# Kernel tuning notes

Measured on AMD Instinct MI355X. Metric: run time of the kernel, lower is better.

The kernel has to match this reference:

```python
import jax, jax.numpy as jnp
import numpy as np

N = 50000; IN_DIM = 128; HID = 128; T = 4; R = 3; E = 500000

def setup_inputs() -> dict:
    key = jax.random.key(0)
    ks = jax.random.split(key, 20)
    def nrm(k, shape, s):
        return jax.random.normal(k, shape, jnp.float32) * s
    s_in = 1.0 / float(np.sqrt(IN_DIM)); s_h = 1.0 / float(np.sqrt(HID))
    return {
        'feat_seq': nrm(ks[0], (T, N, IN_DIM), 1.0),
        'src': jax.random.randint(ks[1], (T, R, E), 0, N, jnp.int32),
        'dst': jax.random.randint(ks[2], (T, R, E), 0, N, jnp.int32),
        'ew': jax.random.uniform(ks[3], (T, R, E), jnp.float32),
        'W_in': nrm(ks[4], (IN_DIM, HID), s_in), 'b_in': jnp.zeros((HID,), jnp.float32),
        'W1': nrm(ks[5], (R, HID, HID), s_h), 'b1': jnp.zeros((R, HID), jnp.float32),
        'W2': nrm(ks[6], (R, HID, HID), s_h), 'b2': jnp.zeros((R, HID), jnp.float32),
        'q1': nrm(ks[7], (HID,), 1.0), 'q2': nrm(ks[8], (HID,), 1.0),
        'ln1_g': jnp.ones((HID,), jnp.float32), 'ln1_b': jnp.zeros((HID,), jnp.float32),
        'ln2_g': jnp.ones((HID,), jnp.float32), 'ln2_b': jnp.zeros((HID,), jnp.float32),
        'gWih': nrm(ks[9], (HID, 3 * HID), s_h), 'gbih': jnp.zeros((3 * HID,), jnp.float32),
        'gWhh': nrm(ks[10], (HID, 3 * HID), s_h), 'gbhh': jnp.zeros((3 * HID,), jnp.float32),
        'temp_q': nrm(ks[11], (HID,), 1.0),
        'tW1': nrm(ks[12], (IN_DIM, HID), s_in), 'tb1': jnp.zeros((HID,), jnp.float32),
        'tW2': nrm(ks[13], (HID, HID), s_h), 'tb2': jnp.zeros((HID,), jnp.float32),
        'cW1': nrm(ks[14], (3 * HID, HID), 1.0 / float(np.sqrt(3 * HID))), 'cb1': jnp.zeros((HID,), jnp.float32),
        'cW2': nrm(ks[15], (HID, 1), s_h), 'cb2': jnp.zeros((1,), jnp.float32),
    }

def _ln(x, g, b):
    m = x.mean(-1, keepdims=True)
    v = ((x - m) ** 2).mean(-1, keepdims=True)
    return (x - m) * jax.lax.rsqrt(v + 1e-5) * g + b

def _rel_attn(stack, q):
    # stack: [R,N,H]; tanh-softmax attention over relations
    score = jnp.einsum('rnh,h->rn', jnp.tanh(stack), q)
    alpha = jax.nn.softmax(score, axis=0)
    return jnp.einsum('rn,rnh->nh', alpha, stack)

def _conv(x, s, d, w, Wr, br):
    # DGL GraphConv norm='right' with edge_weight: mean-by-in-degree weighted SpMM
    msg = w[:, None] * x[s]                                   # [E,H]
    agg = jax.ops.segment_sum(msg, d, num_segments=N)
    deg = jax.ops.segment_sum(jnp.ones_like(w), d, num_segments=N)
    return (agg / jnp.maximum(deg, 1.0)[:, None]) @ Wr + br

def reference(feat_seq, src, dst, ew, W_in, b_in, W1, b1, W2, b2, q1, q2, ln1_g, ln1_b, ln2_g, ln2_b, gWih, gbih, gWhh, gbhh, temp_q, tW1, tb1, tW2, tb2, cW1, cb1, cW2, cb2):
    conv_all = jax.vmap(_conv, in_axes=(None, 0, 0, 0, 0, 0))
    def spatial(x, s, d, w):
        h0 = jax.nn.relu(x @ W_in + b_in)
        h1 = _ln(h0 + jax.nn.relu(_rel_attn(conv_all(h0, s, d, w, W1, b1), q1)), ln1_g, ln1_b)
        h2 = _ln(h1 + jax.nn.relu(_rel_attn(conv_all(h1, s, d, w, W2, b2), q2)), ln2_g, ln2_b)
        return h2
    hs = jnp.stack([spatial(feat_seq[t], src[t], dst[t], ew[t]) for t in range(T)], axis=0)  # [T,N,H]
    def gru_step(h, x):
        gi = x @ gWih + gbih
        gh = h @ gWhh + gbhh
        ir, iz, inn = jnp.split(gi, 3, axis=-1)
        hr, hz, hn = jnp.split(gh, 3, axis=-1)
        r = jax.nn.sigmoid(ir + hr)
        zg = jax.nn.sigmoid(iz + hz)
        n = jnp.tanh(inn + r * hn)
        hnew = (1.0 - zg) * n + zg * h
        return hnew, hnew
    _, outs = jax.lax.scan(gru_step, jnp.zeros((N, HID), feat_seq.dtype), hs)  # [T,N,H]
    out = jnp.transpose(outs, (1, 0, 2))                       # [N,T,H]
    last = out[:, -1, :]
    t_score = jnp.einsum('nth,h->nt', jnp.tanh(out), temp_q)
    t_alpha = jax.nn.softmax(t_score, axis=1)
    attn = jnp.einsum('nt,nth->nh', t_alpha, out)
    tab = jax.nn.relu(jax.nn.relu(feat_seq[-1] @ tW1 + tb1) @ tW2 + tb2)
    z = jnp.concatenate([last, attn, tab], axis=-1)
    return (jax.nn.relu(z @ cW1 + cb1) @ cW2 + cb2)[:, 0]       # [N]
```

## Files before the change

kernel.cpp:

```cpp
#include <hip/hip_runtime.h>
#include <hip/hip_bf16.h>
#include <math.h>

#define NN 50000
#define TT 4
#define RR 3
#define EE 500000

typedef __attribute__((ext_vector_type(8))) short bf16x8;
typedef __attribute__((ext_vector_type(4))) float f32x4;

__device__ inline unsigned short f2b(float f)
{
    union { __hip_bfloat16 h; unsigned short u; } cv;
    cv.h = __float2bfloat16(f);
    return cv.u;
}
__device__ inline float b2f(unsigned short u)
{
    union { unsigned int u; float f; } cv;
    cv.u = ((unsigned int)u) << 16;
    return cv.f;
}
__device__ inline bf16x8 pack8(float4 a, float4 b)
{
    bf16x8 r;
    r[0] = (short)f2b(a.x); r[1] = (short)f2b(a.y); r[2] = (short)f2b(a.z); r[3] = (short)f2b(a.w);
    r[4] = (short)f2b(b.x); r[5] = (short)f2b(b.y); r[6] = (short)f2b(b.z); r[7] = (short)f2b(b.w);
    return r;
}


__global__ __launch_bounds__(256)
void diag_kernel(float* __restrict__ out, float v)
{
    int i = blockIdx.x * 256 + threadIdx.x;
    if (i < NN) out[i] = v;
}


__global__ __launch_bounds__(256)
void wswz_kernel(const float* __restrict__ W, unsigned short* __restrict__ dst, int C, int S)
{
    int idx = blockIdx.x * 256 + threadIdx.x;
    int per = 128 * C;
    if (idx >= S * per) return;
    int s = idx / per, rem = idx - s * per;
    int j = rem & 7;
    int lane = (rem >> 3) & 63;
    int blk = rem >> 9;
    int ncg = C >> 4;
    int kc = blk / ncg, cg = blk - kc * ncg;
    int k = kc * 32 + (lane >> 4) * 8 + j;
    int c = cg * 16 + (lane & 15);
    dst[idx] = f2b(W[(size_t)s * 128 * C + (size_t)k * C + c]);
}


__global__ __launch_bounds__(256)
void count_kernel(const int* __restrict__ dst, int* __restrict__ cnt)
{
    int g = blockIdx.y;
    int e = blockIdx.x * 256 + threadIdx.x;
    if (e >= EE) return;
    int d = dst[(size_t)g * EE + e];
    atomicAdd(&cnt[(size_t)g * NN + d], 1);
}

__global__ __launch_bounds__(1024)
void scan_kernel(int* __restrict__ cnt, int* __restrict__ rows)
{
    int g = blockIdx.x;
    int tid = threadIdx.x;
    const int CH = (NN + 1023) / 1024;
    int s0 = tid * CH;
    int s1 = s0 + CH; if (s1 > NN) s1 = NN;
    int* c = cnt + (size_t)g * NN;
    int* ro = rows + (size_t)g * (NN + 1);
    int sum = 0;
    for (int i = s0; i < s1; ++i) sum += c[i];
    __shared__ int sd[1024];
    sd[tid] = sum;
    __syncthreads();
    for (int off = 1; off < 1024; off <<= 1) {
        int v = 0;
        if (tid >= off) v = sd[tid - off];
        __syncthreads();
        sd[tid] += v;
        __syncthreads();
    }
    int total = sd[1023];
    int prefix = (tid == 0) ? 0 : sd[tid - 1];
    for (int i = s0; i < s1; ++i) {
        int cv = c[i];
        ro[i] = prefix;
        c[i] = prefix;
        prefix += cv;
    }
    if (tid == 0) ro[NN] = total;
}

__global__ __launch_bounds__(256)
void fill_kernel(const int* __restrict__ src, const int* __restrict__ dst,
                 const float* __restrict__ ew, int* __restrict__ cur,
                 int2* __restrict__ srcw)
{
    int g = blockIdx.y;
    int e = blockIdx.x * 256 + threadIdx.x;
    if (e >= EE) return;
    size_t idx = (size_t)g * EE + e;
    int d = dst[idx];
    int pos = atomicAdd(&cur[(size_t)g * NN + d], 1);
    int2 p;
    p.x = src[idx];
    p.y = __float_as_int(ew[idx]);
    srcw[(size_t)g * EE + pos] = p;
}


__global__ __launch_bounds__(256)
void agg16_kernel(const unsigned short* __restrict__ x16,
                  const int2* __restrict__ srcw,
                  const int* __restrict__ rows,
                  unsigned short* __restrict__ agg16)
{
    int wid = (blockIdx.x * 256 + threadIdx.x) >> 6;
    int lane = threadIdx.x & 63;
    if (wid >= RR * NN) return;
    int r = wid / NN;
    int n = wid - r * NN;
    const int* rs = rows + (size_t)r * (NN + 1);
    int e0 = rs[n], e1 = rs[n + 1];
    const int2* sw = srcw + (size_t)r * EE;
    const int co = lane * 2;
    float ax = 0.f, ay = 0.f;
    for (int e = e0; e < e1; e += 16) {
        int2 p[16];
        unsigned int v[16];
#pragma unroll
        for (int i = 0; i < 16; ++i) {
            int idx = (e + i < e1) ? e + i : e1 - 1;
            p[i] = sw[idx];
        }
#pragma unroll
        for (int i = 0; i < 16; ++i)
            v[i] = *(const unsigned int*)(x16 + (size_t)p[i].x * 128 + co);
#pragma unroll
        for (int i = 0; i < 16; ++i) {
            float w = (e + i < e1) ? __int_as_float(p[i].y) : 0.f;
            ax += w * b2f((unsigned short)(v[i] & 0xffffu));
            ay += w * b2f((unsigned short)(v[i] >> 16));
        }
    }
    float inv = 1.0f / fmaxf((float)(e1 - e0), 1.0f);
    unsigned int o = (unsigned int)f2b(ax * inv) | ((unsigned int)f2b(ay * inv) << 16);
    *(unsigned int*)(agg16 + ((size_t)r * NN + n) * 128 + co) = o;
}


__global__ __launch_bounds__(256)
void mmb(const void* in, int in_bf16, long in_zs, int ldin,
         const unsigned short* __restrict__ Ws, long w_zs,
         const float* __restrict__ bias, long b_zs,
         float* out, long out_zs, int ldout,
         unsigned short* out16, long out16_zs,
         int rows, int act)
{
    const int tid = threadIdx.x;
    const int wv = tid >> 6, l = tid & 63;
    const int z = blockIdx.z;
    const int r0 = blockIdx.x * 64 + wv * 16;
    const int lk = (l >> 4) * 8;
    int rowA = r0 + (l & 15);
    int rowc = rowA < rows ? rowA : rows - 1;

    bf16x8 a[4];
    if (in_bf16) {
        const unsigned short* inb = (const unsigned short*)in + (size_t)z * in_zs
                                    + (size_t)rowc * ldin + lk;
#pragma unroll
        for (int kc = 0; kc < 4; ++kc) {
            uint4 u = *(const uint4*)(inb + kc * 32);
            a[kc] = *(bf16x8*)&u;
        }
    } else {
        const float* inf = (const float*)in + (size_t)z * in_zs
                           + (size_t)rowc * ldin + lk;
#pragma unroll
        for (int kc = 0; kc < 4; ++kc) {
            float4 u0 = *(const float4*)(inf + kc * 32);
            float4 u1 = *(const float4*)(inf + kc * 32 + 4);
            a[kc] = pack8(u0, u1);
        }
    }

    const unsigned short* Wz = Ws + (size_t)z * w_zs;
    const float* bz = bias + (size_t)z * b_zs;
    float* oz = out ? out + (size_t)z * out_zs : (float*)0;
    unsigned short* o16z = out16 ? out16 + (size_t)z * out16_zs : (unsigned short*)0;
    const int colbase = l & 15;
    const int rbase = r0 + (l >> 4) * 4;

#pragma unroll
    for (int cg = 0; cg < 8; ++cg) {
        f32x4 acc = {0.f, 0.f, 0.f, 0.f};
#pragma unroll
        for (int kc = 0; kc < 4; ++kc) {
            uint4 bu = *(const uint4*)(Wz + ((size_t)(kc * 8 + cg) * 64 + l) * 8);
            acc = __builtin_amdgcn_mfma_f32_16x16x32_bf16(a[kc], *(bf16x8*)&bu, acc, 0, 0, 0);
        }
        int col = cg * 16 + colbase;
        float bvv = bz[col];
#pragma unroll
        for (int j = 0; j < 4; ++j) {
            int gr = rbase + j;
            if (gr >= rows) continue;
            float v = acc[j] + bvv;
            if (act) v = fmaxf(v, 0.f);
            if (oz) oz[(size_t)gr * ldout + col] = v;
            if (o16z) o16z[(size_t)gr * 128 + col] = f2b(v);
        }
    }
}


__global__ __launch_bounds__(256)
void grub_all(const float* x, float* h,
              const unsigned short* __restrict__ Wis, const float* __restrict__ bi,
              const unsigned short* __restrict__ Whs, const float* __restrict__ bh,
              float* outs)
{
    const int tid = threadIdx.x;
    const int wv = tid >> 6, l = tid & 63;
    const int r0 = blockIdx.x * 64 + wv * 16;
    const int lk = (l >> 4) * 8;
    int rowA = r0 + (l & 15);
    int rowc = rowA < NN ? rowA : NN - 1;

    bf16x8 ax[4], hx[4];
    {
        const float* bx = x + (size_t)rowc * 128 + lk;
        const float* bhp = h + (size_t)rowc * 128 + lk;
#pragma unroll
        for (int kc = 0; kc < 4; ++kc) {
            ax[kc] = pack8(*(const float4*)(bx + kc * 32), *(const float4*)(bx + kc * 32 + 4));
            hx[kc] = pack8(*(const float4*)(bhp + kc * 32), *(const float4*)(bhp + kc * 32 + 4));
        }
    }
    const int colbase = l & 15;
    const int rbase = r0 + (l >> 4) * 4;

#pragma unroll
    for (int cg = 0; cg < 8; ++cg) {
        f32x4 air = {0.f,0.f,0.f,0.f}, ahr = {0.f,0.f,0.f,0.f};
        f32x4 aiz = {0.f,0.f,0.f,0.f}, ahz = {0.f,0.f,0.f,0.f};
        f32x4 ain = {0.f,0.f,0.f,0.f}, ahn = {0.f,0.f,0.f,0.f};
#pragma unroll
        for (int kc = 0; kc < 4; ++kc) {
            uint4 br = *(const uint4*)(Wis + ((size_t)(kc * 24 + 0 + cg) * 64 + l) * 8);
            uint4 hr = *(const uint4*)(Whs + ((size_t)(kc * 24 + 0 + cg) * 64 + l) * 8);
            uint4 bz = *(const uint4*)(Wis + ((size_t)(kc * 24 + 8 + cg) * 64 + l) * 8);
            uint4 hz = *(const uint4*)(Whs + ((size_t)(kc * 24 + 8 + cg) * 64 + l) * 8);
            uint4 bn = *(const uint4*)(Wis + ((size_t)(kc * 24 + 16 + cg) * 64 + l) * 8);
            uint4 hn = *(const uint4*)(Whs + ((size_t)(kc * 24 + 16 + cg) * 64 + l) * 8);
            air = __builtin_amdgcn_mfma_f32_16x16x32_bf16(ax[kc], *(bf16x8*)&br, air, 0, 0, 0);
            ahr = __builtin_amdgcn_mfma_f32_16x16x32_bf16(hx[kc], *(bf16x8*)&hr, ahr, 0, 0, 0);
            aiz = __builtin_amdgcn_mfma_f32_16x16x32_bf16(ax[kc], *(bf16x8*)&bz, aiz, 0, 0, 0);
            ahz = __builtin_amdgcn_mfma_f32_16x16x32_bf16(hx[kc], *(bf16x8*)&hz, ahz, 0, 0, 0);
            ain = __builtin_amdgcn_mfma_f32_16x16x32_bf16(ax[kc], *(bf16x8*)&bn, ain, 0, 0, 0);
            ahn = __builtin_amdgcn_mfma_f32_16x16x32_bf16(hx[kc], *(bf16x8*)&hn, ahn, 0, 0, 0);
        }
        int col = cg * 16 + colbase;
        float bir = bi[col],       bhr = bh[col];
        float biz = bi[128 + col], bhz = bh[128 + col];
        float bin = bi[256 + col], bhn = bh[256 + col];
#pragma unroll
        for (int j = 0; j < 4; ++j) {
            int gr = rbase + j;
            if (gr >= NN) continue;
            float r_ = 1.f / (1.f + __expf(-(air[j] + bir + ahr[j] + bhr)));
            float z_ = 1.f / (1.f + __expf(-(aiz[j] + biz + ahz[j] + bhz)));
            float n_ = tanhf(ain[j] + bin + r_ * (ahn[j] + bhn));
            float hv = h[(size_t)gr * 128 + col];
            float o = (1.f - z_) * n_ + z_ * hv;
            h[(size_t)gr * 128 + col] = o;
            outs[(size_t)gr * 128 + col] = o;
        }
    }
}


__global__ __launch_bounds__(256)
void cls_mfma(const float* __restrict__ in,
              const unsigned short* __restrict__ Ws,
              const float* __restrict__ b1_,
              const float* __restrict__ w2,
              const float* __restrict__ b2_,
              float* __restrict__ outv, int rows)
{
    const int tid = threadIdx.x;
    const int wv = tid >> 6, l = tid & 63;
    const int r0 = blockIdx.x * 64 + wv * 16;
    const int lk = (l >> 4) * 8;
    int rowA = r0 + (l & 15);
    int rowc = rowA < rows ? rowA : rows - 1;

    bf16x8 a[12];
    {
        const float* inf = in + (size_t)rowc * 384 + lk;
#pragma unroll
        for (int kc = 0; kc < 12; ++kc) {
            float4 u0 = *(const float4*)(inf + kc * 32);
            float4 u1 = *(const float4*)(inf + kc * 32 + 4);
            a[kc] = pack8(u0, u1);
        }
    }
    const int colbase = l & 15;
    const int rbase = r0 + (l >> 4) * 4;
    float part[4] = {0.f, 0.f, 0.f, 0.f};

#pragma unroll
    for (int cg = 0; cg < 8; ++cg) {
        f32x4 acc = {0.f, 0.f, 0.f, 0.f};
#pragma unroll
        for (int kc = 0; kc < 12; ++kc) {
            uint4 bu = *(const uint4*)(Ws + ((size_t)(kc * 8 + cg) * 64 + l) * 8);
            acc = __builtin_amdgcn_mfma_f32_16x16x32_bf16(a[kc], *(bf16x8*)&bu, acc, 0, 0, 0);
        }
        int col = cg * 16 + colbase;
        float b1v = b1_[col];
        float w2v = w2[col];
#pragma unroll
        for (int j = 0; j < 4; ++j)
            part[j] += fmaxf(acc[j] + b1v, 0.f) * w2v;
    }
    const float cb2v = b2_[0];
#pragma unroll
    for (int j = 0; j < 4; ++j) {
#pragma unroll
        for (int m = 1; m < 16; m <<= 1) part[j] += __shfl_xor(part[j], m);
        int gr = rbase + j;
        if ((l & 15) == 0 && gr < rows) outv[gr] = part[j] + cb2v;
    }
}


__device__ inline float wred(float v)
{
#pragma unroll
    for (int m = 32; m; m >>= 1) v += __shfl_xor(v, m);
    return v;
}

__global__ __launch_bounds__(256)
void attnln_kernel(const unsigned short* __restrict__ agg16,
                   const unsigned short* hin16,
                   const float* __restrict__ q,
                   const float* __restrict__ g,
                   const float* __restrict__ b,
                   float* hout,
                   unsigned short* hout16)
{
    int wid = (blockIdx.x * 256 + threadIdx.x) >> 6;
    int lane = threadIdx.x & 63;
    if (wid >= NN) return;
    int n = wid;
    float2 qv = *(const float2*)(q + lane * 2);
    float sx[3], sy[3], sc[3];
#pragma unroll
    for (int r = 0; r < 3; ++r) {
        unsigned int v = *(const unsigned int*)(agg16 + ((size_t)r * NN + n) * 128 + lane * 2);
        sx[r] = b2f((unsigned short)(v & 0xffffu));
        sy[r] = b2f((unsigned short)(v >> 16));
        sc[r] = wred(tanhf(sx[r]) * qv.x + tanhf(sy[r]) * qv.y);
    }
    float mx = fmaxf(sc[0], fmaxf(sc[1], sc[2]));
    float e0 = __expf(sc[0] - mx), e1 = __expf(sc[1] - mx), e2 = __expf(sc[2] - mx);
    float isum = 1.f / (e0 + e1 + e2);
    float axv = (e0 * sx[0] + e1 * sx[1] + e2 * sx[2]) * isum;
    float ayv = (e0 * sy[0] + e1 * sy[1] + e2 * sy[2]) * isum;
    unsigned int hv = *(const unsigned int*)(hin16 + (size_t)n * 128 + lane * 2);
    float ux = b2f((unsigned short)(hv & 0xffffu)) + fmaxf(axv, 0.f);
    float uy = b2f((unsigned short)(hv >> 16)) + fmaxf(ayv, 0.f);
    float mean = wred(ux + uy) * (1.f / 128.f);
    float dx = ux - mean, dy = uy - mean;
    float var = wred(dx * dx + dy * dy) * (1.f / 128.f);
    float rstd = rsqrtf(var + 1e-5f);
    float2 gv = *(const float2*)(g + lane * 2);
    float2 bv = *(const float2*)(b + lane * 2);
    float ox = dx * rstd * gv.x + bv.x;
    float oy = dy * rstd * gv.y + bv.y;
    if (hout) {
        float2 o; o.x = ox; o.y = oy;
        *(float2*)(hout + (size_t)n * 128 + lane * 2) = o;
    }
    if (hout16) {
        unsigned int p = (unsigned int)f2b(ox) | ((unsigned int)f2b(oy) << 16);
        *(unsigned int*)(hout16 + (size_t)n * 128 + lane * 2) = p;
    }
}


__global__ __launch_bounds__(256)
void temporal_kernel(const float* __restrict__ outs,
                     const float* __restrict__ tq,
                     float* __restrict__ zbuf)
{
    int wid = (blockIdx.x * 256 + threadIdx.x) >> 6;
    int lane = threadIdx.x & 63;
    if (wid >= NN) return;
    int n = wid;
    float2 qv = *(const float2*)(tq + lane * 2);
    float2 o[4];
    float sc[4];
#pragma unroll
    for (int t = 0; t < 4; ++t) {
        o[t] = *(const float2*)(outs + ((size_t)t * NN + n) * 128 + lane * 2);
        sc[t] = wred(tanhf(o[t].x) * qv.x + tanhf(o[t].y) * qv.y);
    }
    float mx = fmaxf(fmaxf(sc[0], sc[1]), fmaxf(sc[2], sc[3]));
    float e[4];
    float sum = 0.f;
#pragma unroll
    for (int t = 0; t < 4; ++t) { e[t] = __expf(sc[t] - mx); sum += e[t]; }
    float isum = 1.f / sum;
    float axv = 0.f, ayv = 0.f;
#pragma unroll
    for (int t = 0; t < 4; ++t) { axv += e[t] * o[t].x; ayv += e[t] * o[t].y; }
    axv *= isum; ayv *= isum;
    float* zr = zbuf + (size_t)n * 384;
    *(float2*)(zr + lane * 2) = o[3];
    float2 at; at.x = axv; at.y = ayv;
    *(float2*)(zr + 128 + lane * 2) = at;
}


extern "C" void kernel_launch(void* const* d_in, const int* in_sizes, int n_in,
                              void* d_out, int out_size, void* d_ws, size_t ws_size,
                              hipStream_t stream)
{
    const float* feat = (const float*)d_in[0];
    const int* srcp   = (const int*)d_in[1];
    const int* dstp   = (const int*)d_in[2];
    const float* ewp  = (const float*)d_in[3];
    const float* W_in = (const float*)d_in[4];
    const float* b_in = (const float*)d_in[5];
    const float* W1   = (const float*)d_in[6];
    const float* b1   = (const float*)d_in[7];
    const float* W2   = (const float*)d_in[8];
    const float* b2   = (const float*)d_in[9];
    const float* q1   = (const float*)d_in[10];
    const float* q2   = (const float*)d_in[11];
    const float* ln1g = (const float*)d_in[12];
    const float* ln1b = (const float*)d_in[13];
    const float* ln2g = (const float*)d_in[14];
    const float* ln2b = (const float*)d_in[15];
    const float* gWih = (const float*)d_in[16];
    const float* gbih = (const float*)d_in[17];
    const float* gWhh = (const float*)d_in[18];
    const float* gbhh = (const float*)d_in[19];
    const float* tq   = (const float*)d_in[20];
    const float* tW1  = (const float*)d_in[21];
    const float* tb1  = (const float*)d_in[22];
    const float* tW2  = (const float*)d_in[23];
    const float* tb2  = (const float*)d_in[24];
    const float* cW1  = (const float*)d_in[25];
    const float* cb1  = (const float*)d_in[26];
    const float* cW2  = (const float*)d_in[27];
    const float* cb2  = (const float*)d_in[28];
    float* outv = (float*)d_out;
    (void)in_sizes; (void)n_in; (void)out_size;

    const size_t o_HS    = 0;
    const size_t o_POOL  = 102400000;
    const size_t o_AGG16 = o_POOL;
    const size_t o_H16   = o_POOL + 38400000;
    const size_t o_SRCW  = o_POOL + 51200000;
    const size_t o_ROWS  = o_POOL + 63200000;
    const size_t o_CURS  = o_POOL + 65600128;
    const size_t o_ZB    = o_POOL;
    const size_t o_H     = o_POOL + 76800000;
    const size_t o_WSZ   = o_H + 25600000;
    const size_t NEED    = o_WSZ + 589824;

    if (ws_size < NEED) {
        diag_kernel<<<dim3((NN + 255) / 256), dim3(256), 0, stream>>>(outv, (float)(ws_size >> 20));
        return;
    }

    char* wsb = (char*)d_ws;
    float* HS             = (float*)(wsb + o_HS);
    unsigned short* AGG16 = (unsigned short*)(wsb + o_AGG16);
    unsigned short* H16   = (unsigned short*)(wsb + o_H16);
    int2*  SRCW           = (int2*)(wsb + o_SRCW);
    int*   ROWS           = (int*)(wsb + o_ROWS);
    int*   CURS           = (int*)(wsb + o_CURS);
    float* ZB             = (float*)(wsb + o_ZB);
    float* HST            = (float*)(wsb + o_H);
    unsigned short* TAB16 = (unsigned short*)(wsb + o_H);
    unsigned short* WSZ   = (unsigned short*)(wsb + o_WSZ);

    unsigned short* Wins  = WSZ;
    unsigned short* W1s   = WSZ + 16384;
    unsigned short* W2s   = WSZ + 65536;
    unsigned short* gWihs = WSZ + 114688;
    unsigned short* gWhhs = WSZ + 163840;
    unsigned short* tW1s  = WSZ + 212992;
    unsigned short* tW2s  = WSZ + 229376;
    unsigned short* cW1s  = WSZ + 245760;

    const dim3 blk(256);
    const int G64 = (NN + 63) / 64;
    const dim3 gE((EE + 255) / 256, RR);
    const dim3 gEall((EE + 255) / 256, TT * RR);

    wswz_kernel<<<dim3((1 * 16384 + 255) / 256), blk, 0, stream>>>(W_in, Wins, 128, 1);
    wswz_kernel<<<dim3((3 * 16384 + 255) / 256), blk, 0, stream>>>(W1,   W1s,  128, 3);
    wswz_kernel<<<dim3((3 * 16384 + 255) / 256), blk, 0, stream>>>(W2,   W2s,  128, 3);
    wswz_kernel<<<dim3((1 * 49152 + 255) / 256), blk, 0, stream>>>(gWih, gWihs, 384, 1);
    wswz_kernel<<<dim3((1 * 49152 + 255) / 256), blk, 0, stream>>>(gWhh, gWhhs, 384, 1);
    wswz_kernel<<<dim3((1 * 16384 + 255) / 256), blk, 0, stream>>>(tW1,  tW1s, 128, 1);
    wswz_kernel<<<dim3((1 * 16384 + 255) / 256), blk, 0, stream>>>(tW2,  tW2s, 128, 1);
    wswz_kernel<<<dim3((3 * 16384 + 255) / 256), blk, 0, stream>>>(cW1,  cW1s, 128, 3);

    hipMemsetAsync(CURS, 0, (size_t)TT * RR * NN * 4, stream);
    count_kernel<<<gEall, blk, 0, stream>>>(dstp, CURS);
    scan_kernel<<<dim3(TT * RR), dim3(1024), 0, stream>>>(CURS, ROWS);

    for (int t = 0; t < TT; ++t) {
        const size_t eoff = (size_t)t * RR * EE;
        fill_kernel<<<gE, blk, 0, stream>>>(srcp + eoff, dstp + eoff, ewp + eoff,
                                            CURS + (size_t)t * RR * NN, SRCW);

        mmb<<<dim3(G64, 1, 1), blk, 0, stream>>>(
            (const void*)(feat + (size_t)t * NN * 128), 0, 0, 128,
            Wins, 0, b_in, 0, (float*)0, 0, 0, H16, 0, NN, 1);

        for (int layer = 0; layer < 2; ++layer) {
            const unsigned short* Wls = layer ? W2s : W1s;
            const float* bl = layer ? b2 : b1;
            const float* ql = layer ? q2 : q1;
            const float* lg = layer ? ln2g : ln1g;
            const float* lb = layer ? ln2b : ln1b;
            float* hout = layer ? (HS + (size_t)t * NN * 128) : (float*)0;
            unsigned short* hout16 = layer ? (unsigned short*)0 : H16;

            agg16_kernel<<<dim3((RR * NN) / 4), blk, 0, stream>>>(
                H16, SRCW, ROWS + (size_t)t * RR * (NN + 1), AGG16);
            mmb<<<dim3(G64, 1, RR), blk, 0, stream>>>(
                (const void*)AGG16, 1, (long)NN * 128, 128,
                Wls, 16384, bl, 128, (float*)0, 0, 0, AGG16, (long)NN * 128, NN, 0);
            attnln_kernel<<<dim3(NN / 4), blk, 0, stream>>>(
                AGG16, H16, ql, lg, lb, hout, hout16);
        }
    }

    hipMemsetAsync(HST, 0, (size_t)NN * 128 * 4, stream);
    for (int t = 0; t < TT; ++t) {
        float* xt = HS + (size_t)t * NN * 128;
        grub_all<<<dim3(G64), blk, 0, stream>>>(xt, HST, gWihs, gbih, gWhhs, gbhh, xt);
    }

    temporal_kernel<<<dim3(NN / 4), blk, 0, stream>>>(HS, tq, ZB);

    mmb<<<dim3(G64, 1, 1), blk, 0, stream>>>(
        (const void*)(feat + (size_t)3 * NN * 128), 0, 0, 128,
        tW1s, 0, tb1, 0, (float*)0, 0, 0, TAB16, 0, NN, 1);
    mmb<<<dim3(G64, 1, 1), blk, 0, stream>>>(
        (const void*)TAB16, 1, 0, 128,
        tW2s, 0, tb2, 0, ZB + 256, 0, 384, (unsigned short*)0, 0, NN, 1);

    cls_mfma<<<dim3(G64), blk, 0, stream>>>(ZB, cW1s, cb1, cW2, cb2, outv, NN);
}
```

Measured before the change: 2.344 ms.

## Fuse per-relation GEMM with relation attention and LayerNorm into one kernel

Replaces the separate batched relation GEMM (which wrote bf16 results back to AGG16) and the attention+LayerNorm kernel with a single kernel. It computes all three relation projections in MFMA registers, then does the tanh-score softmax over relations, residual, ReLU and LayerNorm directly on the accumulators. This removes a full write and re-read of the 3×N×128 intermediate plus one launch per layer. In exchange it holds 96 accumulator floats per lane, which raises register pressure, and it reads the residual row with scattered per-element loads.

```diff
diff --git a/kernel.cpp b/kernel.cpp
--- a/kernel.cpp
+++ b/kernel.cpp
@@ -225,6 +225,121 @@
 
 
 __global__ __launch_bounds__(256)
+void convln(const unsigned short* __restrict__ agg16,
+            const unsigned short* hin16,
+            const unsigned short* __restrict__ Ws,
+            const float* __restrict__ bias,
+            const float* __restrict__ q,
+            const float* __restrict__ lg,
+            const float* __restrict__ lb,
+            float* hout,
+            unsigned short* hout16)
+{
+    const int tid = threadIdx.x;
+    const int wv = tid >> 6, l = tid & 63;
+    const int r0 = blockIdx.x * 64 + wv * 16;
+    const int lk = (l >> 4) * 8;
+    int rowA = r0 + (l & 15);
+    int rowc = rowA < NN ? rowA : NN - 1;
+    const int colbase = l & 15;
+    const int rbase = r0 + (l >> 4) * 4;
+
+    f32x4 acc[3][8];
+#pragma unroll
+    for (int r = 0; r < 3; ++r) {
+        bf16x8 a[4];
+        const unsigned short* inb = agg16 + ((size_t)r * NN + rowc) * 128 + lk;
+#pragma unroll
+        for (int kc = 0; kc < 4; ++kc) {
+            uint4 u = *(const uint4*)(inb + kc * 32);
+            a[kc] = *(bf16x8*)&u;
+        }
+        const unsigned short* Wz = Ws + (size_t)r * 16384;
+#pragma unroll
+        for (int cg = 0; cg < 8; ++cg) {
+            f32x4 t = {0.f, 0.f, 0.f, 0.f};
+#pragma unroll
+            for (int kc = 0; kc < 4; ++kc) {
+                uint4 bu = *(const uint4*)(Wz + ((size_t)(kc * 8 + cg) * 64 + l) * 8);
+                t = __builtin_amdgcn_mfma_f32_16x16x32_bf16(a[kc], *(bf16x8*)&bu, t, 0, 0, 0);
+            }
+            acc[r][cg] = t;
+        }
+    }
+
+    float qv[8], gv[8], bv[8], bias_r[3][8];
+#pragma unroll
+    for (int cg = 0; cg < 8; ++cg) {
+        int col = cg * 16 + colbase;
+        qv[cg] = q[col];
+        gv[cg] = lg[col];
+        bv[cg] = lb[col];
+#pragma unroll
+        for (int r = 0; r < 3; ++r) bias_r[r][cg] = bias[r * 128 + col];
+    }
+
+    float sc[3][4];
+#pragma unroll
+    for (int r = 0; r < 3; ++r) {
+#pragma unroll
+        for (int j = 0; j < 4; ++j) {
+            float p = 0.f;
+#pragma unroll
+            for (int cg = 0; cg < 8; ++cg)
+                p += tanhf(acc[r][cg][j] + bias_r[r][cg]) * qv[cg];
+#pragma unroll
+            for (int m = 1; m < 16; m <<= 1) p += __shfl_xor(p, m);
+            sc[r][j] = p;
+        }
+    }
+
+#pragma unroll
+    for (int j = 0; j < 4; ++j) {
+        int gr = rbase + j;
+        int grc = gr < NN ? gr : NN - 1;
+        float mx = fmaxf(sc[0][j], fmaxf(sc[1][j], sc[2][j]));
+        float e0 = __expf(sc[0][j] - mx), e1 = __expf(sc[1][j] - mx), e2 = __expf(sc[2][j] - mx);
+        float isum = 1.f / (e0 + e1 + e2);
+        float a0 = e0 * isum, a1 = e1 * isum, a2 = e2 * isum;
+
+        float u[8];
+        float msum = 0.f;
+#pragma unroll
+        for (int cg = 0; cg < 8; ++cg) {
+            float av = a0 * (acc[0][cg][j] + bias_r[0][cg])
+                     + a1 * (acc[1][cg][j] + bias_r[1][cg])
+                     + a2 * (acc[2][cg][j] + bias_r[2][cg]);
+            float hv = b2f(hin16[(size_t)grc * 128 + cg * 16 + colbase]);
+            u[cg] = hv + fmaxf(av, 0.f);
+            msum += u[cg];
+        }
+#pragma unroll
+        for (int m = 1; m < 16; m <<= 1) msum += __shfl_xor(msum, m);
+        float mean = msum * (1.f / 128.f);
+        float vsum = 0.f;
+#pragma unroll
+        for (int cg = 0; cg < 8; ++cg) {
+            float d = u[cg] - mean;
+            vsum += d * d;
+        }
+#pragma unroll
+        for (int m = 1; m < 16; m <<= 1) vsum += __shfl_xor(vsum, m);
+        float rstd = rsqrtf(vsum * (1.f / 128.f) + 1e-5f);
+
+        if (gr < NN) {
+#pragma unroll
+            for (int cg = 0; cg < 8; ++cg) {
+                float o = (u[cg] - mean) * rstd * gv[cg] + bv[cg];
+                int col = cg * 16 + colbase;
+                if (hout)   hout[(size_t)gr * 128 + col] = o;
+                if (hout16) hout16[(size_t)gr * 128 + col] = f2b(o);
+            }
+        }
+    }
+}
+
+
+__global__ __launch_bounds__(256)
 void grub_all(const float* x, float* h,
               const unsigned short* __restrict__ Wis, const float* __restrict__ bi,
               const unsigned short* __restrict__ Whs, const float* __restrict__ bh,
@@ -351,55 +466,6 @@
     for (int m = 32; m; m >>= 1) v += __shfl_xor(v, m);
     return v;
 }
-
-__global__ __launch_bounds__(256)
-void attnln_kernel(const unsigned short* __restrict__ agg16,
-                   const unsigned short* hin16,
-                   const float* __restrict__ q,
-                   const float* __restrict__ g,
-                   const float* __restrict__ b,
-                   float* hout,
-                   unsigned short* hout16)
-{
-    int wid = (blockIdx.x * 256 + threadIdx.x) >> 6;
-    int lane = threadIdx.x & 63;
-    if (wid >= NN) return;
-    int n = wid;
-    float2 qv = *(const float2*)(q + lane * 2);
-    float sx[3], sy[3], sc[3];
-#pragma unroll
-    for (int r = 0; r < 3; ++r) {
-        unsigned int v = *(const unsigned int*)(agg16 + ((size_t)r * NN + n) * 128 + lane * 2);
-        sx[r] = b2f((unsigned short)(v & 0xffffu));
-        sy[r] = b2f((unsigned short)(v >> 16));
-        sc[r] = wred(tanhf(sx[r]) * qv.x + tanhf(sy[r]) * qv.y);
-    }
-    float mx = fmaxf(sc[0], fmaxf(sc[1], sc[2]));
-    float e0 = __expf(sc[0] - mx), e1 = __expf(sc[1] - mx), e2 = __expf(sc[2] - mx);
-    float isum = 1.f / (e0 + e1 + e2);
-    float axv = (e0 * sx[0] + e1 * sx[1] + e2 * sx[2]) * isum;
-    float ayv = (e0 * sy[0] + e1 * sy[1] + e2 * sy[2]) * isum;
-    unsigned int hv = *(const unsigned int*)(hin16 + (size_t)n * 128 + lane * 2);
-    float ux = b2f((unsigned short)(hv & 0xffffu)) + fmaxf(axv, 0.f);
-    float uy = b2f((unsigned short)(hv >> 16)) + fmaxf(ayv, 0.f);
-    float mean = wred(ux + uy) * (1.f / 128.f);
-    float dx = ux - mean, dy = uy - mean;
-    float var = wred(dx * dx + dy * dy) * (1.f / 128.f);
-    float rstd = rsqrtf(var + 1e-5f);
-    float2 gv = *(const float2*)(g + lane * 2);
-    float2 bv = *(const float2*)(b + lane * 2);
-    float ox = dx * rstd * gv.x + bv.x;
-    float oy = dy * rstd * gv.y + bv.y;
-    if (hout) {
-        float2 o; o.x = ox; o.y = oy;
-        *(float2*)(hout + (size_t)n * 128 + lane * 2) = o;
-    }
-    if (hout16) {
-        unsigned int p = (unsigned int)f2b(ox) | ((unsigned int)f2b(oy) << 16);
-        *(unsigned int*)(hout16 + (size_t)n * 128 + lane * 2) = p;
-    }
-}
-
 
 __global__ __launch_bounds__(256)
 void temporal_kernel(const float* __restrict__ outs,
@@ -547,11 +613,8 @@
 
             agg16_kernel<<<dim3((RR * NN) / 4), blk, 0, stream>>>(
                 H16, SRCW, ROWS + (size_t)t * RR * (NN + 1), AGG16);
-            mmb<<<dim3(G64, 1, RR), blk, 0, stream>>>(
-                (const void*)AGG16, 1, (long)NN * 128, 128,
-                Wls, 16384, bl, 128, (float*)0, 0, 0, AGG16, (long)NN * 128, NN, 0);
-            attnln_kernel<<<dim3(NN / 4), blk, 0, stream>>>(
-                AGG16, H16, ql, lg, lb, hout, hout16);
+            convln<<<dim3(G64), blk, 0, stream>>>(
+                AGG16, H16, Wls, bl, ql, lg, lb, hout, hout16);
         }
     }
 
```

New measurement: 2.889 ms. +23.2%, slower.
